# Performance work log

Measured on AMD Instinct MI355X. Metric: run time of the kernel, lower is better.

## Reference

```python
import jax, jax.numpy as jnp
import numpy as np

SCALE = 30.0
MARGIN = 0.5
COS_M = float(np.cos(MARGIN))
SIN_M = float(np.sin(MARGIN))
TH = float(np.cos(np.pi - MARGIN))
MM = float(np.sin(np.pi - MARGIN) * MARGIN)
LN_EPS = 1e-7

B, S, H = 16, 2048, 1024
N_SPANS = 64
N_CLASSES = 4096


def setup_inputs() -> dict:
    key = jax.random.key(0)
    k1, k2, k3, k4, k5 = jax.random.split(key, 5)
    encoder_layer = jax.random.normal(k1, (B, S, H), dtype=jnp.float32)
    ln_gamma = jnp.ones((H,), jnp.float32)
    ln_beta = jnp.zeros((H,), jnp.float32)
    # xavier-uniform-like init for arcface head weight [out, in]
    limit = float(np.sqrt(6.0 / (N_CLASSES + H)))
    arc_weight = jax.random.uniform(k2, (N_CLASSES, H), jnp.float32, -limit, limit)
    heads = jax.random.randint(k3, (B, N_SPANS), 0, S - 32).astype(jnp.int32)
    lens = jax.random.randint(k4, (B, N_SPANS), 1, 33).astype(jnp.int32)
    tails = heads + lens  # guaranteed head < tail <= S
    labels = jax.random.randint(k5, (B, N_SPANS), 0, N_CLASSES).astype(jnp.int32)
    return {
        "encoder_layer": encoder_layer,
        "ln_gamma": ln_gamma,
        "ln_beta": ln_beta,
        "arc_weight": arc_weight,
        "span_head_idxs": heads,
        "span_tail_idxs": tails,
        "labels": labels,
    }


def _span_mean(encoder_layer, heads, tails):
    # fused ragged segment-mean via inclusive prefix sums over the seq dim
    # csum: [B, S+1, H], csum[b, t] = sum of encoder_layer[b, :t]
    csum = jnp.concatenate(
        [jnp.zeros_like(encoder_layer[:, :1]), jnp.cumsum(encoder_layer, axis=1)], axis=1
    )
    gather = lambda idx: jnp.take_along_axis(csum, idx[:, :, None].astype(jnp.int32), axis=1)
    sums = gather(tails) - gather(heads)  # [B, n_spans, H]
    counts = (tails - heads).astype(encoder_layer.dtype)[:, :, None]
    return sums / counts


def _layer_norm(x, gamma, beta):
    mu = jnp.mean(x, axis=-1, keepdims=True)
    var = jnp.mean(jnp.square(x - mu), axis=-1, keepdims=True)
    return (x - mu) * jax.lax.rsqrt(var + LN_EPS) * gamma + beta


def _l2norm(x):
    return x / jnp.maximum(jnp.linalg.norm(x, axis=-1, keepdims=True), 1e-12)


def reference(encoder_layer, ln_gamma, ln_beta, arc_weight, span_head_idxs, span_tail_idxs, labels):
    emb = _span_mean(encoder_layer, span_head_idxs, span_tail_idxs)  # [B, n_spans, H]
    emb = _layer_norm(emb, ln_gamma, ln_beta)
    emb = emb.reshape(-1, emb.shape[-1])  # [B*n_spans, H]
    lab = labels.reshape(-1)
    # ArcMarginProduct: cosine similarity
    cosine = (_l2norm(emb) @ _l2norm(arc_weight).T).astype(jnp.float32)  # [N, C]
    sine = jnp.sqrt(jnp.clip(1.0 - jnp.square(cosine), 0.0))
    phi = cosine * COS_M - sine * SIN_M
    phi = jnp.where(cosine > TH, phi, cosine - MM)
    onehot = jax.nn.one_hot(lab, cosine.shape[-1], dtype=cosine.dtype)
    logits = (onehot * phi + (1.0 - onehot) * cosine) * SCALE
    # mean cross entropy (all labels valid, ignore_index unused)
    logp = jax.nn.log_softmax(logits, axis=-1)
    nll = -jnp.take_along_axis(logp, lab[:, None].astype(jnp.int32), axis=1)[:, 0]
    return jnp.mean(nll)
```

## Files before the change

kernel.cpp:

```cpp
#include <hip/hip_runtime.h>
#include <hip/hip_bf16.h>
#include <math.h>

#define B_     16
#define S_     2048
#define H_     1024
#define NS_    64
#define NC_    4096
#define NROWS  1024

#define SCALE_ 30.0f
#define COS_M_ 0.8775825618903728f
#define SIN_M_ 0.479425538604203f
#define TH_    (-0.8775825618903728f)
#define MM_    0.2397127693021015f
#define LN_EPS_ 1e-7f


__device__ __forceinline__ unsigned short f2bf(float f) {
    union { float f; unsigned int u; } v; v.f = f;
    unsigned int r = v.u + 0x7fffu + ((v.u >> 16) & 1u);
    return (unsigned short)(r >> 16);
}

__device__ __forceinline__ float block_sum(float v) {
    __shared__ float sb[4];
    #pragma unroll
    for (int off = 32; off > 0; off >>= 1) v += __shfl_down(v, off, 64);
    if ((threadIdx.x & 63) == 0) sb[threadIdx.x >> 6] = v;
    __syncthreads();
    float r = sb[0] + sb[1] + sb[2] + sb[3];
    __syncthreads();
    return r;
}

__device__ __forceinline__ void gload16(const void* g, void* l) {
    __builtin_amdgcn_global_load_lds(
        (const __attribute__((address_space(1))) unsigned int*)g,
        (__attribute__((address_space(3))) unsigned int*)l,
        16, 0, 0);
}

typedef short bf16x8 __attribute__((ext_vector_type(8)));
typedef float f32x4  __attribute__((ext_vector_type(4)));

__global__ __launch_bounds__(256) void prep_kernel(
    const float* __restrict__ enc,
    const float* __restrict__ gamma,
    const float* __restrict__ beta,
    const float* __restrict__ W,
    const int*   __restrict__ heads,
    const int*   __restrict__ tails,
    unsigned short* __restrict__ embn,
    unsigned short* __restrict__ Wn)
{
    const int tid = threadIdx.x;
    if (blockIdx.x >= NROWS) {
        const int row = blockIdx.x - NROWS;
        float4 x = ((const float4*)(W + (size_t)row * H_))[tid];
        float ss = block_sum(x.x*x.x + x.y*x.y + x.z*x.z + x.w*x.w);
        float invn = 1.0f / fmaxf(sqrtf(ss), 1e-12f);
        ushort4 o;
        o.x = f2bf(x.x * invn); o.y = f2bf(x.y * invn);
        o.z = f2bf(x.z * invn); o.w = f2bf(x.w * invn);
        *(ushort4*)(Wn + (size_t)row * H_ + tid * 4) = o;
        return;
    }
    const int span = blockIdx.x;
    const int b    = span >> 6;
    const int head = heads[span];
    const int tail = tails[span];
    const int cnt  = tail - head;

    const float4* base = (const float4*)(enc + ((size_t)b * S_ + head) * H_);
    float4 a; a.x = 0.f; a.y = 0.f; a.z = 0.f; a.w = 0.f;
    for (int s = 0; s < cnt; ++s) {
        float4 x = base[s * (H_ / 4) + tid];
        a.x += x.x; a.y += x.y; a.z += x.z; a.w += x.w;
    }
    const float inv = 1.0f / (float)cnt;
    float v0 = a.x * inv, v1 = a.y * inv, v2 = a.z * inv, v3 = a.w * inv;

    float mu = block_sum(v0 + v1 + v2 + v3) * (1.0f / H_);
    float d0 = v0 - mu, d1 = v1 - mu, d2 = v2 - mu, d3 = v3 - mu;
    float var = block_sum(d0*d0 + d1*d1 + d2*d2 + d3*d3) * (1.0f / H_);
    float rstd = rsqrtf(var + LN_EPS_);

    const int h = tid * 4;
    float y0 = d0 * rstd * gamma[h+0] + beta[h+0];
    float y1 = d1 * rstd * gamma[h+1] + beta[h+1];
    float y2 = d2 * rstd * gamma[h+2] + beta[h+2];
    float y3 = d3 * rstd * gamma[h+3] + beta[h+3];

    float ss = block_sum(y0*y0 + y1*y1 + y2*y2 + y3*y3);
    float invn = 1.0f / fmaxf(sqrtf(ss), 1e-12f);

    ushort4 o;
    o.x = f2bf(y0 * invn); o.y = f2bf(y1 * invn);
    o.z = f2bf(y2 * invn); o.w = f2bf(y3 * invn);
    *(ushort4*)(embn + (size_t)span * H_ + h) = o;
}

__global__ __launch_bounds__(256) void gemm_arc_kernel(
    const unsigned short* __restrict__ A,
    const unsigned short* __restrict__ Bw,
    const int*   __restrict__ labels,
    float* __restrict__ pmax,
    float* __restrict__ psum,
    float* __restrict__ labval)
{
    __shared__ short As[64 * 32];
    __shared__ short Bs[128 * 32];
    __shared__ float red_m[2][64];
    __shared__ float red_s[2][64];

    const int m0   = blockIdx.x * 64;
    const int n0   = blockIdx.y * 128;
    const int nb   = blockIdx.y;
    const int tid  = threadIdx.x;
    const int lane = tid & 63;
    const int w    = tid >> 6;
    const int wm   = (w & 1) * 32;
    const int wn   = (w >> 1) * 64;
    const int lrow = lane & 15;
    const int q    = lane >> 4;

    const int rowA   = tid >> 2;
    const int kchunk = (tid & 3) * 8;

    f32x4 acc[2][4];
    #pragma unroll
    for (int i = 0; i < 2; ++i)
        #pragma unroll
        for (int j = 0; j < 4; ++j)
            acc[i][j] = (f32x4){0.f, 0.f, 0.f, 0.f};

    for (int k0 = 0; k0 < 1024; k0 += 32) {
        __syncthreads();
        gload16(A + ((size_t)(m0 + rowA) * 1024 + k0 + kchunk), &As[rowA * 32 + kchunk]);
        #pragma unroll
        for (int t = 0; t < 2; ++t) {
            const int r = t * 64 + rowA;
            gload16(Bw + ((size_t)(n0 + r) * 1024 + k0 + kchunk), &Bs[r * 32 + kchunk]);
        }
        __syncthreads();

        bf16x8 af[2], bfr[4];
        #pragma unroll
        for (int i = 0; i < 2; ++i)
            af[i] = *(const bf16x8*)(&As[(wm + i * 16 + lrow) * 32 + q * 8]);
        #pragma unroll
        for (int j = 0; j < 4; ++j)
            bfr[j] = *(const bf16x8*)(&Bs[(wn + j * 16 + lrow) * 32 + q * 8]);

        #pragma unroll
        for (int i = 0; i < 2; ++i)
            #pragma unroll
            for (int j = 0; j < 4; ++j)
                acc[i][j] = __builtin_amdgcn_mfma_f32_16x16x32_bf16(af[i], bfr[j], acc[i][j], 0, 0, 0);
    }

    #pragma unroll
    for (int i = 0; i < 2; ++i) {
        #pragma unroll
        for (int r2 = 0; r2 < 4; ++r2) {
            const int rloc = wm + i * 16 + q * 4 + r2;
            const int grow = m0 + rloc;
            const int lab  = labels[grow];
            float lg[4];
            float lm = -1e30f;
            #pragma unroll
            for (int j = 0; j < 4; ++j) {
                float c = acc[i][j][r2];
                const int gcol = n0 + wn + j * 16 + lrow;
                float logit = c * SCALE_;
                if (gcol == lab) {
                    float sine = sqrtf(fmaxf(1.0f - c * c, 0.0f));
                    float phi  = c * COS_M_ - sine * SIN_M_;
                    float pl   = (c > TH_) ? phi : (c - MM_);
                    logit = pl * SCALE_;
                    labval[grow] = logit;
                }
                lg[j] = logit;
                lm = fmaxf(lm, logit);
            }
            float ls = 0.f;
            #pragma unroll
            for (int j = 0; j < 4; ++j) ls += expf(lg[j] - lm);
            #pragma unroll
            for (int d = 1; d < 16; d <<= 1) {
                float om = __shfl_xor(lm, d, 64);
                float os = __shfl_xor(ls, d, 64);
                float nm = fmaxf(lm, om);
                ls = ls * expf(lm - nm) + os * expf(om - nm);
                lm = nm;
            }
            if (lrow == 0) { red_m[w >> 1][rloc] = lm; red_s[w >> 1][rloc] = ls; }
        }
    }
    __syncthreads();
    if (tid < 64) {
        float ma = red_m[0][tid], sa = red_s[0][tid];
        float mb = red_m[1][tid], sb = red_s[1][tid];
        float M = fmaxf(ma, mb);
        float S = sa * expf(ma - M) + sb * expf(mb - M);
        pmax[(size_t)nb * NROWS + m0 + tid] = M;
        psum[(size_t)nb * NROWS + m0 + tid] = S;
    }
}

__global__ __launch_bounds__(1024) void finalize_kernel(
    const float* __restrict__ pmax,
    const float* __restrict__ psum,
    const float* __restrict__ labval,
    float* __restrict__ out)
{
    __shared__ float sb[16];
    const int row = threadIdx.x;
    float m = pmax[row], s = psum[row];
    #pragma unroll 4
    for (int nbk = 1; nbk < 32; ++nbk) {
        float om = pmax[nbk * NROWS + row];
        float os = psum[nbk * NROWS + row];
        float nm = fmaxf(m, om);
        s = s * expf(m - nm) + os * expf(om - nm);
        m = nm;
    }
    float nll = logf(s) + m - labval[row];
    #pragma unroll
    for (int off = 32; off > 0; off >>= 1) nll += __shfl_down(nll, off, 64);
    if ((row & 63) == 0) sb[row >> 6] = nll;
    __syncthreads();
    if (row < 64) {
        float v = (row < 16) ? sb[row] : 0.f;
        #pragma unroll
        for (int off = 8; off > 0; off >>= 1) v += __shfl_down(v, off, 64);
        if (row == 0) out[0] = v * (1.0f / NROWS);
    }
}

extern "C" void kernel_launch(void* const* d_in, const int* in_sizes, int n_in,
                              void* d_out, int out_size, void* d_ws, size_t ws_size,
                              hipStream_t stream) {
    const float* enc    = (const float*)d_in[0];
    const float* gamma  = (const float*)d_in[1];
    const float* beta   = (const float*)d_in[2];
    const float* W      = (const float*)d_in[3];
    const int*   heads  = (const int*)d_in[4];
    const int*   tails  = (const int*)d_in[5];
    const int*   labels = (const int*)d_in[6];
    float* out = (float*)d_out;

    char* ws = (char*)d_ws;
    unsigned short* embn   = (unsigned short*)(ws);
    unsigned short* Wn     = (unsigned short*)(ws + (2u  << 20));
    float*          pmax   = (float*)        (ws + (10u << 20));
    float*          psum   = (float*)        (ws + (10u << 20) + (128u << 10));
    float*          labval = (float*)        (ws + (10u << 20) + (256u << 10));

    prep_kernel<<<NROWS + NC_, 256, 0, stream>>>(enc, gamma, beta, W, heads, tails, embn, Wn);
    dim3 g2(NROWS / 64, NC_ / 128);
    gemm_arc_kernel<<<g2, 256, 0, stream>>>(embn, Wn, labels, pmax, psum, labval);
    finalize_kernel<<<1, 1024, 0, stream>>>(pmax, psum, labval, out);
}
```

Before: 236.3 us.

## Fuse finalize into GEMM via atomic ticket, widen K-tile with swizzled LDS

Removes the separate finalize kernel: each GEMM block takes an atomic ticket after writing its partials, and the last block does the cross-block log-sum-exp reduction and writes the loss. The GEMM K-step goes from 32 to 64 with an XOR-swizzled LDS layout to cut bank conflicts and halve the number of barriers. The grid is flattened to 1D with a remapped block order. The counter is reset in the prep kernel. The tail reduction now runs on a single 256-thread block instead of 1024 threads, which may lengthen it.

```diff
diff --git a/kernel.cpp b/kernel.cpp
--- a/kernel.cpp
+++ b/kernel.cpp
@@ -52,7 +52,8 @@
     const int*   __restrict__ heads,
     const int*   __restrict__ tails,
     unsigned short* __restrict__ embn,
-    unsigned short* __restrict__ Wn)
+    unsigned short* __restrict__ Wn,
+    unsigned int* __restrict__ counter)
 {
     const int tid = threadIdx.x;
     if (blockIdx.x >= NROWS) {
@@ -66,6 +67,7 @@
         *(ushort4*)(Wn + (size_t)row * H_ + tid * 4) = o;
         return;
     }
+    if (blockIdx.x == 0 && tid == 0) *counter = 0u;
     const int span = blockIdx.x;
     const int b    = span >> 6;
     const int head = heads[span];
@@ -107,16 +109,21 @@
     const int*   __restrict__ labels,
     float* __restrict__ pmax,
     float* __restrict__ psum,
-    float* __restrict__ labval)
+    float* __restrict__ labval,
+    unsigned int* __restrict__ counter,
+    float* __restrict__ out)
 {
-    __shared__ short As[64 * 32];
-    __shared__ short Bs[128 * 32];
+    __shared__ short As[64 * 64];
+    __shared__ short Bs[128 * 64];
     __shared__ float red_m[2][64];
     __shared__ float red_s[2][64];
-
-    const int m0   = blockIdx.x * 64;
-    const int n0   = blockIdx.y * 128;
-    const int nb   = blockIdx.y;
+    __shared__ unsigned int s_tkt;
+
+    const int id   = blockIdx.x;
+    const int bx   = id >> 5;
+    const int by   = id & 31;
+    const int m0   = bx * 64;
+    const int n0   = by * 128;
     const int tid  = threadIdx.x;
     const int lane = tid & 63;
     const int w    = tid >> 6;
@@ -125,9 +132,6 @@
     const int lrow = lane & 15;
     const int q    = lane >> 4;
 
-    const int rowA   = tid >> 2;
-    const int kchunk = (tid & 3) * 8;
-
     f32x4 acc[2][4];
     #pragma unroll
     for (int i = 0; i < 2; ++i)
@@ -135,29 +139,48 @@
         for (int j = 0; j < 4; ++j)
             acc[i][j] = (f32x4){0.f, 0.f, 0.f, 0.f};
 
-    for (int k0 = 0; k0 < 1024; k0 += 32) {
+    for (int k0 = 0; k0 < 1024; k0 += 64) {
         __syncthreads();
-        gload16(A + ((size_t)(m0 + rowA) * 1024 + k0 + kchunk), &As[rowA * 32 + kchunk]);
-        #pragma unroll
-        for (int t = 0; t < 2; ++t) {
-            const int r = t * 64 + rowA;
-            gload16(Bw + ((size_t)(n0 + r) * 1024 + k0 + kchunk), &Bs[r * 32 + kchunk]);
+        #pragma unroll
+        for (int p = 0; p < 2; ++p) {
+            const int c   = p * 256 + tid;
+            const int row = c >> 3;
+            const int g   = (c & 7) ^ (row & 7);
+            gload16(A + ((size_t)(m0 + row) << 10) + k0 + g * 8, &As[c * 8]);
+        }
+        #pragma unroll
+        for (int p = 0; p < 4; ++p) {
+            const int c   = p * 256 + tid;
+            const int row = c >> 3;
+            const int g   = (c & 7) ^ (row & 7);
+            gload16(Bw + ((size_t)(n0 + row) << 10) + k0 + g * 8, &Bs[c * 8]);
         }
         __syncthreads();
 
-        bf16x8 af[2], bfr[4];
-        #pragma unroll
-        for (int i = 0; i < 2; ++i)
-            af[i] = *(const bf16x8*)(&As[(wm + i * 16 + lrow) * 32 + q * 8]);
-        #pragma unroll
-        for (int j = 0; j < 4; ++j)
-            bfr[j] = *(const bf16x8*)(&Bs[(wn + j * 16 + lrow) * 32 + q * 8]);
-
-        #pragma unroll
-        for (int i = 0; i < 2; ++i)
-            #pragma unroll
-            for (int j = 0; j < 4; ++j)
-                acc[i][j] = __builtin_amdgcn_mfma_f32_16x16x32_bf16(af[i], bfr[j], acc[i][j], 0, 0, 0);
+        bf16x8 af[2][2], bfr[2][4];
+        #pragma unroll
+        for (int ks = 0; ks < 2; ++ks) {
+            #pragma unroll
+            for (int i = 0; i < 2; ++i) {
+                const int r   = wm + i * 16 + lrow;
+                const int pos = (ks * 4 + q) ^ (r & 7);
+                af[ks][i] = *(const bf16x8*)(&As[r * 64 + pos * 8]);
+            }
+            #pragma unroll
+            for (int j = 0; j < 4; ++j) {
+                const int r   = wn + j * 16 + lrow;
+                const int pos = (ks * 4 + q) ^ (r & 7);
+                bfr[ks][j] = *(const bf16x8*)(&Bs[r * 64 + pos * 8]);
+            }
+        }
+        #pragma unroll
+        for (int ks = 0; ks < 2; ++ks)
+            #pragma unroll
+            for (int i = 0; i < 2; ++i)
+                #pragma unroll
+                for (int j = 0; j < 4; ++j)
+                    acc[i][j] = __builtin_amdgcn_mfma_f32_16x16x32_bf16(
+                        af[ks][i], bfr[ks][j], acc[i][j], 0, 0, 0);
     }
 
     #pragma unroll
@@ -204,39 +227,32 @@
         float mb = red_m[1][tid], sb = red_s[1][tid];
         float M = fmaxf(ma, mb);
         float S = sa * expf(ma - M) + sb * expf(mb - M);
-        pmax[(size_t)nb * NROWS + m0 + tid] = M;
-        psum[(size_t)nb * NROWS + m0 + tid] = S;
-    }
-}
-
-__global__ __launch_bounds__(1024) void finalize_kernel(
-    const float* __restrict__ pmax,
-    const float* __restrict__ psum,
-    const float* __restrict__ labval,
-    float* __restrict__ out)
-{
-    __shared__ float sb[16];
-    const int row = threadIdx.x;
-    float m = pmax[row], s = psum[row];
-    #pragma unroll 4
-    for (int nbk = 1; nbk < 32; ++nbk) {
-        float om = pmax[nbk * NROWS + row];
-        float os = psum[nbk * NROWS + row];
-        float nm = fmaxf(m, om);
-        s = s * expf(m - nm) + os * expf(om - nm);
-        m = nm;
-    }
-    float nll = logf(s) + m - labval[row];
-    #pragma unroll
-    for (int off = 32; off > 0; off >>= 1) nll += __shfl_down(nll, off, 64);
-    if ((row & 63) == 0) sb[row >> 6] = nll;
-    __syncthreads();
-    if (row < 64) {
-        float v = (row < 16) ? sb[row] : 0.f;
-        #pragma unroll
-        for (int off = 8; off > 0; off >>= 1) v += __shfl_down(v, off, 64);
-        if (row == 0) out[0] = v * (1.0f / NROWS);
-    }
+        pmax[(size_t)by * NROWS + m0 + tid] = M;
+        psum[(size_t)by * NROWS + m0 + tid] = S;
+    }
+
+    __threadfence();
+    __syncthreads();
+    if (tid == 0) s_tkt = atomicAdd(counter, 1u);
+    __syncthreads();
+    if (s_tkt != 511u) return;
+    __threadfence();
+
+    float local = 0.f;
+    for (int rr = tid; rr < NROWS; rr += 256) {
+        float m = pmax[rr], s = psum[rr];
+        #pragma unroll 4
+        for (int nbk = 1; nbk < 32; ++nbk) {
+            float om = pmax[(size_t)nbk * NROWS + rr];
+            float os = psum[(size_t)nbk * NROWS + rr];
+            float nm = fmaxf(m, om);
+            s = s * expf(m - nm) + os * expf(om - nm);
+            m = nm;
+        }
+        local += logf(s) + m - labval[rr];
+    }
+    float tot = block_sum(local);
+    if (tid == 0) out[0] = tot * (1.0f / NROWS);
 }
 
 extern "C" void kernel_launch(void* const* d_in, const int* in_sizes, int n_in,
@@ -252,14 +268,15 @@
     float* out = (float*)d_out;
 
     char* ws = (char*)d_ws;
-    unsigned short* embn   = (unsigned short*)(ws);
-    unsigned short* Wn     = (unsigned short*)(ws + (2u  << 20));
-    float*          pmax   = (float*)        (ws + (10u << 20));
-    float*          psum   = (float*)        (ws + (10u << 20) + (128u << 10));
-    float*          labval = (float*)        (ws + (10u << 20) + (256u << 10));
-
-    prep_kernel<<<NROWS + NC_, 256, 0, stream>>>(enc, gamma, beta, W, heads, tails, embn, Wn);
-    dim3 g2(NROWS / 64, NC_ / 128);
-    gemm_arc_kernel<<<g2, 256, 0, stream>>>(embn, Wn, labels, pmax, psum, labval);
-    finalize_kernel<<<1, 1024, 0, stream>>>(pmax, psum, labval, out);
-}
+    unsigned short* embn    = (unsigned short*)(ws);
+    unsigned short* Wn      = (unsigned short*)(ws + (2u  << 20));
+    float*          pmax    = (float*)        (ws + (10u << 20));
+    float*          psum    = (float*)        (ws + (10u << 20) + (128u << 10));
+    float*          labval  = (float*)        (ws + (10u << 20) + (256u << 10));
+    unsigned int*   counter = (unsigned int*) (ws + (10u << 20) + (260u << 10));
+
+    prep_kernel<<<NROWS + NC_, 256, 0, stream>>>(enc, gamma, beta, W, heads, tails,
+                                                 embn, Wn, counter);
+    gemm_arc_kernel<<<512, 256, 0, stream>>>(embn, Wn, labels, pmax, psum, labval,
+                                             counter, out);
+}
```

Result: slower. 282.4 us (+19.5%).
